# Kernel tuning notes

Measured on AMD Instinct MI355X. Metric: run time of the kernel, lower is better.

## Reference

```python
import jax, jax.numpy as jnp
import numpy as np

HIDDEN = 768
NUM_BLOCKS = 8
BLOCK = HIDDEN // NUM_BLOCKS
BASE_THR, K_DECAY, MIN_THR = 0.01, 20.0, 0.0005


def _threshold(height, width):
    # wavenumber-dependent soft-shrink threshold T(k), shape [H, W//2+1]
    fu = jnp.fft.fftfreq(height, d=1.0).astype(jnp.float32)[:, None]
    fv = jnp.fft.rfftfreq(width, d=1.0).astype(jnp.float32)[None, :]
    k = jnp.sqrt(fu ** 2 + fv ** 2) * max(height, width)
    thr = BASE_THR * jnp.exp(-0.5 * (k / K_DECAY) ** 2)
    return jnp.maximum(thr, MIN_THR)


def setup_inputs() -> dict:
    key = jax.random.key(0)
    kx, k1, k2, k3, k4 = jax.random.split(key, 5)
    scale = 0.02
    x = jax.random.normal(kx, (4, 128, 128, HIDDEN), dtype=jnp.float32)
    w1 = scale * jax.random.normal(k1, (2, NUM_BLOCKS, BLOCK, BLOCK), dtype=jnp.float32)
    b1 = scale * jax.random.normal(k2, (2, NUM_BLOCKS, BLOCK), dtype=jnp.float32)
    w2 = scale * jax.random.normal(k3, (2, NUM_BLOCKS, BLOCK, BLOCK), dtype=jnp.float32)
    b2 = scale * jax.random.normal(k4, (2, NUM_BLOCKS, BLOCK), dtype=jnp.float32)
    return {"x": x, "w1": w1, "b1": b1, "w2": w2, "b2": b2}


def reference(x, w1, b1, w2, b2):
    dtype = x.dtype
    bias = x
    xf = x.astype(jnp.float32)
    B, H, W, C = xf.shape
    Wc = W // 2 + 1
    # rfft2 over spatial dims, orthonormal
    Xc = jnp.fft.rfft2(xf, axes=(1, 2), norm='ortho')
    Xc = Xc.reshape(B, H, Wc, NUM_BLOCKS, BLOCK)
    xr, xi = jnp.real(Xc), jnp.imag(Xc)
    mm = lambda t, w: jnp.einsum('bhwni,nio->bhwno', t, w)
    # complex block-diagonal 2-layer MLP
    o1r = jax.nn.relu(mm(xr, w1[0]) - mm(xi, w1[1]) + b1[0])
    o1i = jax.nn.relu(mm(xi, w1[0]) + mm(xr, w1[1]) + b1[1])
    o2r = mm(o1r, w2[0]) - mm(o1i, w2[1]) + b2[0]
    o2i = mm(o1i, w2[0]) + mm(o1r, w2[1]) + b2[1]
    # soft-shrink on complex magnitude with wavenumber-dependent threshold
    mag = jnp.sqrt(o2r ** 2 + o2i ** 2 + 1e-8)
    thr = _threshold(H, W)[None, :, :, None, None]  # [1,H,Wc,1,1]
    sf = jax.nn.relu(mag - thr) / mag
    Yc = (o2r * sf) + 1j * (o2i * sf)
    Yc = Yc.reshape(B, H, Wc, C)
    y = jnp.fft.irfft2(Yc, s=(H, W), axes=(1, 2), norm='ortho')
    return y.astype(dtype) + bias
```

## Files before the change

### kernel.cpp

```cpp
#include <hip/hip_runtime.h>
#include <hip/hip_bf16.h>
#include <math.h>


#define HD   768
#define NBLK 8
#define HH   128
#define WW   128
#define WC   65
#define NPOS (HH * WC)

constexpr float SC    = 0.08838834764831845f;
constexpr float TWOPI = 6.28318530717958647692f;

constexpr int TM_OFF     = 0;
constexpr int TW_OFF     = 49152;
constexpr int TWI_OFF    = 69632;
constexpr int WF_OFF     = 90112;
constexpr int WF_END_U16 = 679936;
constexpr size_t A_UINTS = (size_t)4 * NPOS * HD;

typedef __attribute__((ext_vector_type(8))) short short8;
typedef __attribute__((ext_vector_type(4))) float f32x4;

#define MFMA __builtin_amdgcn_mfma_f32_16x16x32_bf16

static __device__ inline unsigned short f2bf(float f) {
  __hip_bfloat16 h = __float2bfloat16(f);
  return __builtin_bit_cast(unsigned short, h);
}
static __device__ inline unsigned int pack2(float re, float im) {
  return (unsigned int)f2bf(re) | ((unsigned int)f2bf(im) << 16);
}

__global__ __launch_bounds__(256) void k_prep(const float* __restrict__ w1,
                                              const float* __restrict__ b1,
                                              const float* __restrict__ w2,
                                              const float* __restrict__ b2,
                                              unsigned short* __restrict__ wf,
                                              float* __restrict__ bpk) {
  const int blk = blockIdx.x, t = threadIdx.x;
  if (blk < 16) {
    const int layer = blk >> 3, n = blk & 7;
    const float* w  = layer ? w2 : w1;
    const float* bs = layer ? b2 : b1;
    unsigned short* dst = wf + WF_OFF + (size_t)blk * (72 * 512);
    for (int e = t; e < 72 * 512; e += 256) {
      int f = e >> 9, idx = e & 511;
      int kk = f / 12, nt = f - kk * 12;
      int lane = idx >> 3, j = idx & 7;
      int k  = kk * 32 + (lane >> 4) * 8 + j;
      int cc = nt * 16 + (lane & 15);
      float v;
      if (k < 96) v = (cc < 96) ? w[(size_t)n * 9216 + k * 96 + cc]
                                : w[(size_t)(8 + n) * 9216 + k * 96 + (cc - 96)];
      else        v = (cc < 96) ? -w[(size_t)(8 + n) * 9216 + (k - 96) * 96 + cc]
                                :  w[(size_t)n * 9216 + (k - 96) * 96 + (cc - 96)];
      dst[e] = f2bf(v);
    }
    for (int c = t; c < 192; c += 256)
      bpk[blk * 192 + c] = (c < 96) ? bs[n * 96 + c] : bs[(8 + n) * 96 + (c - 96)];
  } else if (blk == 16) {
    for (int e = t; e < 96 * 512; e += 256) {
      int f = e >> 9, idx = e & 511;
      int part = f >> 5, rem = f & 31, kot = rem >> 2, kk = rem & 3;
      int lane = idx >> 3, j = idx & 7;
      int ko = kot * 16 + (lane & 15);
      int r  = kk * 32 + (lane >> 4) * 8 + j;
      float sn, cs; sincosf((TWOPI / 128.f) * (float)((ko * r) & 127), &sn, &cs);
      float v = (part == 0) ? cs : (part == 1) ? sn : -sn;
      wf[TM_OFF + (size_t)f * 512 + idx] = f2bf(v * SC);
    }
  } else if (blk == 17) {
    for (int e = t; e < 40 * 512; e += 256) {
      int f = e >> 9, idx = e & 511;
      int mt = f >> 2, kk = f & 3;
      int lane = idx >> 3, j = idx & 7;
      int row = mt * 16 + (lane & 15);
      int r   = kk * 32 + (lane >> 4) * 8 + j;
      int kor = (row < 80) ? row : row - 80;
      float sn, cs; sincosf((TWOPI / 128.f) * (float)((kor * r) & 127), &sn, &cs);
      wf[TW_OFF + (size_t)f * 512 + idx] = f2bf((row < 80 ? cs : -sn) * SC);
    }
  } else {
    for (int e = t; e < 40 * 512; e += 256) {
      int f = e >> 9, idx = e & 511;
      int mt = f / 5, kk = f - mt * 5;
      int lane = idx >> 3, j = idx & 7;
      int wr = mt * 16 + (lane & 15);
      int k  = kk * 32 + (lane >> 4) * 8 + j;
      float v = 0.f;
      if (k < 80) {
        int kb = k;
        if (kb <= 64) {
          float sn, cs; sincosf((TWOPI / 128.f) * (float)((wr * kb) & 127), &sn, &cs);
          v = SC * ((kb == 0 || kb == 64) ? 1.f : 2.f) * cs;
        }
      } else {
        int kb = k - 80;
        if (kb >= 1 && kb <= 63) {
          float sn, cs; sincosf((TWOPI / 128.f) * (float)((wr * kb) & 127), &sn, &cs);
          v = -2.f * SC * sn;
        }
      }
      wf[TWI_OFF + (size_t)f * 512 + idx] = f2bf(v);
    }
  }
}

__global__ __launch_bounds__(256) void k_fft_w(const float* __restrict__ x,
                                               unsigned int* __restrict__ A,
                                               const unsigned short* __restrict__ wf) {
  __shared__ unsigned short Xt[64 * 136];
  const int h = blockIdx.x, c0 = blockIdx.y * 64, b = blockIdx.z, t = threadIdx.x;
  const int wv = t >> 6, lane = t & 63, l15 = lane & 15, lg = lane >> 4;
  const float* xp = x + ((size_t)(b * HH + h)) * WW * HD + c0;
  for (int idx = t; idx < 128 * 64; idx += 256) {
    int r = idx >> 6, ch = idx & 63;
    Xt[ch * 136 + r] = f2bf(xp[(size_t)r * HD + ch]);
  }
  __syncthreads();
  const unsigned short* tw = wf + TW_OFF;
  f32x4 acc[10];
#pragma unroll
  for (int m = 0; m < 10; ++m) acc[m] = { 0.f, 0.f, 0.f, 0.f };
#pragma unroll
  for (int kk = 0; kk < 4; ++kk) {
    short8 bq = *(const short8*)&Xt[(wv * 16 + l15) * 136 + kk * 32 + lg * 8];
#pragma unroll
    for (int m = 0; m < 10; ++m) {
      short8 a = *(const short8*)&tw[(size_t)(m * 4 + kk) * 512 + lane * 8];
      acc[m] = MFMA(a, bq, acc[m], 0, 0, 0);
    }
  }
  unsigned int* Ao = A + ((size_t)b * NPOS + h * WC) * HD + c0 + wv * 16 + l15;
#pragma unroll
  for (int q = 0; q < 5; ++q)
#pragma unroll
    for (int r = 0; r < 4; ++r) {
      int ko = q * 16 + lg * 4 + r;
      if (ko <= 64) Ao[(size_t)ko * HD] = pack2(acc[q][r], acc[5 + q][r]);
    }
}

__global__ __launch_bounds__(256) void k_ifft_w(const unsigned int* __restrict__ A,
                                                const float* __restrict__ x,
                                                float* __restrict__ out,
                                                const unsigned short* __restrict__ wf) {
  __shared__ unsigned short Zt[64 * 168];
  const int h = blockIdx.x, c0 = blockIdx.y * 64, b = blockIdx.z, t = threadIdx.x;
  const int wv = t >> 6, lane = t & 63, l15 = lane & 15, lg = lane >> 4;
  const unsigned int* Ai = A + ((size_t)b * NPOS + h * WC) * HD + c0;
  for (int idx = t; idx < 65 * 64; idx += 256) {
    int kb = idx >> 6, ch = idx & 63;
    unsigned int u = Ai[(size_t)kb * HD + ch];
    Zt[ch * 168 + kb]      = (unsigned short)(u & 0xffffu);
    Zt[ch * 168 + 80 + kb] = (unsigned short)(u >> 16);
  }
  for (int idx = t; idx < 64 * 32; idx += 256) {
    int ch = idx >> 5, q = idx & 31;
    if (q < 30) {
      int kb = 65 + (q % 15), half = q / 15;
      Zt[ch * 168 + half * 80 + kb] = 0;
    }
  }
  __syncthreads();
  const unsigned short* twi = wf + TWI_OFF;
  f32x4 acc[8];
#pragma unroll
  for (int m = 0; m < 8; ++m) acc[m] = { 0.f, 0.f, 0.f, 0.f };
#pragma unroll
  for (int kk = 0; kk < 5; ++kk) {
    short8 bq = *(const short8*)&Zt[(wv * 16 + l15) * 168 + kk * 32 + lg * 8];
#pragma unroll
    for (int m = 0; m < 8; ++m) {
      short8 a = *(const short8*)&twi[(size_t)(m * 5 + kk) * 512 + lane * 8];
      acc[m] = MFMA(a, bq, acc[m], 0, 0, 0);
    }
  }
#pragma unroll
  for (int m = 0; m < 8; ++m)
#pragma unroll
    for (int r = 0; r < 4; ++r) {
      int wr = m * 16 + lg * 4 + r;
      size_t go = (((size_t)(b * HH + h)) * WW + wr) * HD + c0 + wv * 16 + l15;
      out[go] = acc[m][r] + x[go];
    }
}

template <int FWD>
static __device__ inline void dft_gemm16(const unsigned short* Rb, const unsigned short* Ib,
                                         const unsigned short* tm, int rt, int cb, int lane,
                                         f32x4* aR, f32x4* aI) {
  const int l15 = lane & 15, lg = lane >> 4;
#pragma unroll
  for (int kkr = 0; kkr < 4; ++kkr) {
    const int r0 = kkr * 32 + lg * 8;
    short8 Ac = *(const short8*)&tm[(size_t)(0 * 32 + rt * 4 + kkr) * 512 + lane * 8];
    short8 As = *(const short8*)&tm[(size_t)(1 * 32 + rt * 4 + kkr) * 512 + lane * 8];
    short8 An = *(const short8*)&tm[(size_t)(2 * 32 + rt * 4 + kkr) * 512 + lane * 8];
#pragma unroll
    for (int c = 0; c < 3; ++c) {
      short8 zr = *(const short8*)&Rb[((cb + c) * 16 + l15) * 136 + r0];
      short8 zi = *(const short8*)&Ib[((cb + c) * 16 + l15) * 136 + r0];
      aR[c] = MFMA(Ac, zr, aR[c], 0, 0, 0);
      if constexpr (FWD) {
        aR[c] = MFMA(As, zi, aR[c], 0, 0, 0);
        aI[c] = MFMA(Ac, zi, aI[c], 0, 0, 0);
        aI[c] = MFMA(An, zr, aI[c], 0, 0, 0);
      } else {
        aR[c] = MFMA(An, zi, aR[c], 0, 0, 0);
        aI[c] = MFMA(Ac, zi, aI[c], 0, 0, 0);
        aI[c] = MFMA(As, zr, aI[c], 0, 0, 0);
      }
    }
  }
}

__global__ __launch_bounds__(1024) void k_mid(unsigned int* __restrict__ A,
                                              const unsigned short* __restrict__ wf,
                                              const float* __restrict__ bpk) {
  __shared__ unsigned short Rb[13312], Ib[13312];
  __shared__ unsigned short WfL[36 * 512];
  const int kv = blockIdx.x, n = blockIdx.y, b = blockIdx.z, t = threadIdx.x;
  const int w = t >> 6, lane = t & 63, l15 = lane & 15, lg = lane >> 4;
  const int rt = w >> 1, cb = (w & 1) * 3;
  unsigned int* Abase = A + ((size_t)b * NPOS + kv) * HD + n * 96;
  const unsigned short* tm = wf + TM_OFF;

  for (int idx = t; idx < 128 * 96; idx += 1024) {
    int r = idx / 96, ch = idx - r * 96;
    unsigned int u = Abase[(size_t)r * (WC * HD) + ch];
    Rb[ch * 136 + r] = (unsigned short)(u & 0xffffu);
    Ib[ch * 136 + r] = (unsigned short)(u >> 16);
  }
  {
    const int4* s1 = (const int4*)(wf + WF_OFF + (size_t)n * (72 * 512));
    for (int idx = t; idx < 2304; idx += 1024) ((int4*)WfL)[idx] = s1[idx];
  }
  __syncthreads();

  f32x4 aR[3], aI[3];
#pragma unroll
  for (int c = 0; c < 3; ++c) { aR[c] = {0.f,0.f,0.f,0.f}; aI[c] = {0.f,0.f,0.f,0.f}; }
  dft_gemm16<1>(Rb, Ib, tm, rt, cb, lane, aR, aI);
  __syncthreads();
#pragma unroll
  for (int c = 0; c < 3; ++c)
#pragma unroll
    for (int r = 0; r < 4; ++r) {
      int row = rt * 16 + lg * 4 + r, ch = (cb + c) * 16 + l15;
      Rb[row * 104 + ch] = f2bf(aR[c][r]);
      Ib[row * 104 + ch] = f2bf(aI[c][r]);
    }
  __syncthreads();

  const int row_a = (rt * 16 + l15) * 104;
  f32x4 acc[6];
#pragma unroll
  for (int i = 0; i < 3; ++i) {
    float bv = bpk[n * 192 + (cb + i) * 16 + l15];
    acc[i] = { bv, bv, bv, bv };
    bv = bpk[n * 192 + (cb + i + 6) * 16 + l15];
    acc[3 + i] = { bv, bv, bv, bv };
  }
#pragma unroll
  for (int kk = 0; kk < 6; ++kk) {
    short8 a = (kk < 3) ? *(const short8*)&Rb[row_a + kk * 32 + lg * 8]
                        : *(const short8*)&Ib[row_a + (kk - 3) * 32 + lg * 8];
#pragma unroll
    for (int i = 0; i < 6; ++i) {
      int nt = cb + (i < 3 ? i : i + 3);
      short8 bfr;
      if (kk < 3) bfr = *(const short8*)&WfL[(kk * 12 + nt) * 512 + lane * 8];
      else {
        int nt2 = (nt < 6) ? nt + 6 : nt - 6;
        int4 nb = *(const int4*)&WfL[((kk - 3) * 12 + nt2) * 512 + lane * 8];
        if (nt < 6) { nb.x ^= 0x80008000; nb.y ^= 0x80008000; nb.z ^= 0x80008000; nb.w ^= 0x80008000; }
        bfr = __builtin_bit_cast(short8, nb);
      }
      acc[i] = MFMA(a, bfr, acc[i], 0, 0, 0);
    }
  }
  __syncthreads();
#pragma unroll
  for (int i = 0; i < 3; ++i)
#pragma unroll
    for (int r = 0; r < 4; ++r) {
      int row = rt * 16 + lg * 4 + r, ch = (cb + i) * 16 + l15;
      Rb[row * 104 + ch] = f2bf(fmaxf(acc[i][r], 0.f));
      Ib[row * 104 + ch] = f2bf(fmaxf(acc[3 + i][r], 0.f));
    }
  {
    const int4* s2 = (const int4*)(wf + WF_OFF + (size_t)(8 + n) * (72 * 512));
    for (int idx = t; idx < 2304; idx += 1024) ((int4*)WfL)[idx] = s2[idx];
  }
  __syncthreads();

#pragma unroll
  for (int i = 0; i < 3; ++i) {
    float bv = bpk[(8 + n) * 192 + (cb + i) * 16 + l15];
    acc[i] = { bv, bv, bv, bv };
    bv = bpk[(8 + n) * 192 + (cb + i + 6) * 16 + l15];
    acc[3 + i] = { bv, bv, bv, bv };
  }
#pragma unroll
  for (int kk = 0; kk < 6; ++kk) {
    short8 a = (kk < 3) ? *(const short8*)&Rb[row_a + kk * 32 + lg * 8]
                        : *(const short8*)&Ib[row_a + (kk - 3) * 32 + lg * 8];
#pragma unroll
    for (int i = 0; i < 6; ++i) {
      int nt = cb + (i < 3 ? i : i + 3);
      short8 bfr;
      if (kk < 3) bfr = *(const short8*)&WfL[(kk * 12 + nt) * 512 + lane * 8];
      else {
        int nt2 = (nt < 6) ? nt + 6 : nt - 6;
        int4 nb = *(const int4*)&WfL[((kk - 3) * 12 + nt2) * 512 + lane * 8];
        if (nt < 6) { nb.x ^= 0x80008000; nb.y ^= 0x80008000; nb.z ^= 0x80008000; nb.w ^= 0x80008000; }
        bfr = __builtin_bit_cast(short8, nb);
      }
      acc[i] = MFMA(a, bfr, acc[i], 0, 0, 0);
    }
  }
  __syncthreads();

#pragma unroll
  for (int r = 0; r < 4; ++r) {
    int ko = rt * 16 + lg * 4 + r;
    float kus = (ko >= 64) ? (float)(ko - 128) : (float)ko;
    float k2v = kus * kus + (float)(kv * kv);
    float thr = fmaxf(0.01f * expf(-0.00125f * k2v), 0.0005f);
#pragma unroll
    for (int i = 0; i < 3; ++i) {
      float mr = acc[i][r], mi = acc[3 + i][r];
      float mag = sqrtf(mr * mr + mi * mi + 1e-8f);
      float sf = fmaxf(mag - thr, 0.f) / mag;
      int ch = (cb + i) * 16 + l15;
      Rb[ch * 136 + ko] = f2bf(mr * sf);
      Ib[ch * 136 + ko] = f2bf(mi * sf);
    }
  }
  __syncthreads();

#pragma unroll
  for (int c = 0; c < 3; ++c) { aR[c] = {0.f,0.f,0.f,0.f}; aI[c] = {0.f,0.f,0.f,0.f}; }
  dft_gemm16<0>(Rb, Ib, tm, rt, cb, lane, aR, aI);
#pragma unroll
  for (int c = 0; c < 3; ++c)
#pragma unroll
    for (int r = 0; r < 4; ++r) {
      int rr = rt * 16 + lg * 4 + r, ch = (cb + c) * 16 + l15;
      Abase[(size_t)rr * (WC * HD) + ch] = pack2(aR[c][r], aI[c][r]);
    }
}

extern "C" void kernel_launch(void* const* d_in, const int* in_sizes, int n_in,
                              void* d_out, int out_size, void* d_ws, size_t ws_size,
                              hipStream_t stream) {
  const float* x  = (const float*)d_in[0];
  const float* w1 = (const float*)d_in[1];
  const float* b1 = (const float*)d_in[2];
  const float* w2 = (const float*)d_in[3];
  const float* b2 = (const float*)d_in[4];
  float* out = (float*)d_out;
  unsigned int* A = (unsigned int*)d_ws;

  unsigned short* wf = (unsigned short*)(A + A_UINTS);
  float* bpk = (float*)(wf + WF_END_U16);

  k_prep<<<19, 256, 0, stream>>>(w1, b1, w2, b2, wf, bpk);
  k_fft_w<<<dim3(HH, HD / 64, 4), 256, 0, stream>>>(x, A, wf);
  k_mid<<<dim3(WC, NBLK, 4), 1024, 0, stream>>>(A, wf, bpk);
  k_ifft_w<<<dim3(HH, HD / 64, 4), 256, 0, stream>>>(A, x, out, wf);
}
```

Baseline: 462.3 us.

## Fold residual add into spectrum and double-buffer MLP weight tiles in k_mid

The residual x is no longer read in fp32 at the inverse FFT. Instead k_mid writes its filtered spectrum to a separate buffer, and k_ifft_w adds it to the stored forward spectrum of x before the inverse transform. This uses linearity of the orthonormal rfft/irfft pair and saves a full-size fp32 read of x, at the cost of one extra bf16-complex read and reconstructing x from a bf16 spectrum, which can lose accuracy. k_mid also streams its MLP weights through two 12-tile LDS buffers overlapped with compute, instead of loading all 36 tiles up front. It packs pairs of rows into 32-bit LDS stores and adds a launch-bounds occupancy hint.

```diff
diff --git a/kernel.cpp b/kernel.cpp
--- a/kernel.cpp
+++ b/kernel.cpp
@@ -31,6 +31,12 @@
 }
 static __device__ inline unsigned int pack2(float re, float im) {
   return (unsigned int)f2bf(re) | ((unsigned int)f2bf(im) << 16);
+}
+static __device__ inline float lo2f(unsigned int u) {
+  return __builtin_bit_cast(float, u << 16);
+}
+static __device__ inline float hi2f(unsigned int u) {
+  return __builtin_bit_cast(float, u & 0xffff0000u);
 }
 
 __global__ __launch_bounds__(256) void k_prep(const float* __restrict__ w1,
@@ -144,18 +150,21 @@
 }
 
 __global__ __launch_bounds__(256) void k_ifft_w(const unsigned int* __restrict__ A,
-                                                const float* __restrict__ x,
+                                                const unsigned int* __restrict__ Bp,
                                                 float* __restrict__ out,
                                                 const unsigned short* __restrict__ wf) {
   __shared__ unsigned short Zt[64 * 168];
   const int h = blockIdx.x, c0 = blockIdx.y * 64, b = blockIdx.z, t = threadIdx.x;
   const int wv = t >> 6, lane = t & 63, l15 = lane & 15, lg = lane >> 4;
-  const unsigned int* Ai = A + ((size_t)b * NPOS + h * WC) * HD + c0;
+  const size_t base = ((size_t)b * NPOS + h * WC) * HD + c0;
   for (int idx = t; idx < 65 * 64; idx += 256) {
     int kb = idx >> 6, ch = idx & 63;
-    unsigned int u = Ai[(size_t)kb * HD + ch];
-    Zt[ch * 168 + kb]      = (unsigned short)(u & 0xffffu);
-    Zt[ch * 168 + 80 + kb] = (unsigned short)(u >> 16);
+    unsigned int uA = A[base + (size_t)kb * HD + ch];
+    unsigned int uB = Bp[base + (size_t)kb * HD + ch];
+    float re = lo2f(uA) + lo2f(uB);
+    float im = hi2f(uA) + hi2f(uB);
+    Zt[ch * 168 + kb]      = f2bf(re);
+    Zt[ch * 168 + 80 + kb] = (kb == 0 || kb == 64) ? (unsigned short)0 : f2bf(im);
   }
   for (int idx = t; idx < 64 * 32; idx += 256) {
     int ch = idx >> 5, q = idx & 31;
@@ -184,7 +193,7 @@
     for (int r = 0; r < 4; ++r) {
       int wr = m * 16 + lg * 4 + r;
       size_t go = (((size_t)(b * HH + h)) * WW + wr) * HD + c0 + wv * 16 + l15;
-      out[go] = acc[m][r] + x[go];
+      out[go] = acc[m][r];
     }
 }
 
@@ -217,26 +226,31 @@
   }
 }
 
-__global__ __launch_bounds__(1024) void k_mid(unsigned int* __restrict__ A,
-                                              const unsigned short* __restrict__ wf,
-                                              const float* __restrict__ bpk) {
+__global__ __launch_bounds__(1024, 8) void k_mid(const unsigned int* __restrict__ A,
+                                                 unsigned int* __restrict__ Bp,
+                                                 const unsigned short* __restrict__ wf,
+                                                 const float* __restrict__ bpk) {
   __shared__ unsigned short Rb[13312], Ib[13312];
-  __shared__ unsigned short WfL[36 * 512];
+  __shared__ unsigned short WfX[2][12 * 512];
   const int kv = blockIdx.x, n = blockIdx.y, b = blockIdx.z, t = threadIdx.x;
   const int w = t >> 6, lane = t & 63, l15 = lane & 15, lg = lane >> 4;
   const int rt = w >> 1, cb = (w & 1) * 3;
-  unsigned int* Abase = A + ((size_t)b * NPOS + kv) * HD + n * 96;
+  const size_t pbase = ((size_t)b * NPOS + kv) * HD + n * 96;
   const unsigned short* tm = wf + TM_OFF;
-
-  for (int idx = t; idx < 128 * 96; idx += 1024) {
-    int r = idx / 96, ch = idx - r * 96;
-    unsigned int u = Abase[(size_t)r * (WC * HD) + ch];
-    Rb[ch * 136 + r] = (unsigned short)(u & 0xffffu);
-    Ib[ch * 136 + r] = (unsigned short)(u >> 16);
-  }
+  const unsigned short* wf1 = wf + WF_OFF + (size_t)n * (72 * 512);
+  const unsigned short* wf2 = wf + WF_OFF + (size_t)(8 + n) * (72 * 512);
+
   {
-    const int4* s1 = (const int4*)(wf + WF_OFF + (size_t)n * (72 * 512));
-    for (int idx = t; idx < 2304; idx += 1024) ((int4*)WfL)[idx] = s1[idx];
+    unsigned int* Rb32 = (unsigned int*)Rb;
+    unsigned int* Ib32 = (unsigned int*)Ib;
+    for (int idx = t; idx < 64 * 96; idx += 1024) {
+      int r2 = idx / 96, ch = idx - r2 * 96;
+      unsigned int u0 = A[pbase + (size_t)(2 * r2) * (WC * HD) + ch];
+      unsigned int u1 = A[pbase + (size_t)(2 * r2 + 1) * (WC * HD) + ch];
+      Rb32[ch * 68 + r2] = (u0 & 0xffffu) | (u1 << 16);
+      Ib32[ch * 68 + r2] = (u0 >> 16) | (u1 & 0xffff0000u);
+    }
+    if (t < 768) ((int4*)WfX[0])[t] = ((const int4*)(wf1 + 0 * 12 * 512))[t];
   }
   __syncthreads();
 
@@ -244,7 +258,9 @@
 #pragma unroll
   for (int c = 0; c < 3; ++c) { aR[c] = {0.f,0.f,0.f,0.f}; aI[c] = {0.f,0.f,0.f,0.f}; }
   dft_gemm16<1>(Rb, Ib, tm, rt, cb, lane, aR, aI);
-  __syncthreads();
+  if (t < 768) ((int4*)WfX[1])[t] = ((const int4*)(wf1 + 1 * 12 * 512))[t];
+  __syncthreads();
+
 #pragma unroll
   for (int c = 0; c < 3; ++c)
 #pragma unroll
@@ -264,25 +280,33 @@
     bv = bpk[n * 192 + (cb + i + 6) * 16 + l15];
     acc[3 + i] = { bv, bv, bv, bv };
   }
-#pragma unroll
-  for (int kk = 0; kk < 6; ++kk) {
-    short8 a = (kk < 3) ? *(const short8*)&Rb[row_a + kk * 32 + lg * 8]
-                        : *(const short8*)&Ib[row_a + (kk - 3) * 32 + lg * 8];
-#pragma unroll
-    for (int i = 0; i < 6; ++i) {
-      int nt = cb + (i < 3 ? i : i + 3);
-      short8 bfr;
-      if (kk < 3) bfr = *(const short8*)&WfL[(kk * 12 + nt) * 512 + lane * 8];
-      else {
-        int nt2 = (nt < 6) ? nt + 6 : nt - 6;
-        int4 nb = *(const int4*)&WfL[((kk - 3) * 12 + nt2) * 512 + lane * 8];
-        if (nt < 6) { nb.x ^= 0x80008000; nb.y ^= 0x80008000; nb.z ^= 0x80008000; nb.w ^= 0x80008000; }
-        bfr = __builtin_bit_cast(short8, nb);
-      }
-      acc[i] = MFMA(a, bfr, acc[i], 0, 0, 0);
-    }
-  }
-  __syncthreads();
+
+#define MLP_PAIR(k0, BUF)                                                        \
+  {                                                                              \
+    short8 aRf = *(const short8*)&Rb[row_a + (k0) * 32 + lg * 8];                \
+    short8 aIf = *(const short8*)&Ib[row_a + (k0) * 32 + lg * 8];                \
+    _Pragma("unroll")                                                            \
+    for (int i = 0; i < 6; ++i) {                                                \
+      int nt = cb + (i < 3 ? i : i + 3);                                         \
+      short8 b0 = *(const short8*)&(BUF)[nt * 512 + lane * 8];                   \
+      acc[i] = MFMA(aRf, b0, acc[i], 0, 0, 0);                                   \
+      int nt2 = (nt < 6) ? nt + 6 : nt - 6;                                      \
+      int4 nb = *(const int4*)&(BUF)[nt2 * 512 + lane * 8];                      \
+      if (nt < 6) { nb.x ^= 0x80008000; nb.y ^= 0x80008000;                      \
+                    nb.z ^= 0x80008000; nb.w ^= 0x80008000; }                    \
+      acc[i] = MFMA(aIf, __builtin_bit_cast(short8, nb), acc[i], 0, 0, 0);       \
+    }                                                                            \
+  }
+
+  MLP_PAIR(0, WfX[0]);
+  __syncthreads();
+  MLP_PAIR(1, WfX[1]);
+  if (t < 768) ((int4*)WfX[0])[t] = ((const int4*)(wf1 + 2 * 12 * 512))[t];
+  __syncthreads();
+  MLP_PAIR(2, WfX[0]);
+  if (t < 768) ((int4*)WfX[1])[t] = ((const int4*)(wf2 + 0 * 12 * 512))[t];
+  __syncthreads();
+
 #pragma unroll
   for (int i = 0; i < 3; ++i)
 #pragma unroll
@@ -291,10 +315,7 @@
       Rb[row * 104 + ch] = f2bf(fmaxf(acc[i][r], 0.f));
       Ib[row * 104 + ch] = f2bf(fmaxf(acc[3 + i][r], 0.f));
     }
-  {
-    const int4* s2 = (const int4*)(wf + WF_OFF + (size_t)(8 + n) * (72 * 512));
-    for (int idx = t; idx < 2304; idx += 1024) ((int4*)WfL)[idx] = s2[idx];
-  }
+  if (t < 768) ((int4*)WfX[0])[t] = ((const int4*)(wf2 + 1 * 12 * 512))[t];
   __syncthreads();
 
 #pragma unroll
@@ -304,24 +325,12 @@
     bv = bpk[(8 + n) * 192 + (cb + i + 6) * 16 + l15];
     acc[3 + i] = { bv, bv, bv, bv };
   }
-#pragma unroll
-  for (int kk = 0; kk < 6; ++kk) {
-    short8 a = (kk < 3) ? *(const short8*)&Rb[row_a + kk * 32 + lg * 8]
-                        : *(const short8*)&Ib[row_a + (kk - 3) * 32 + lg * 8];
-#pragma unroll
-    for (int i = 0; i < 6; ++i) {
-      int nt = cb + (i < 3 ? i : i + 3);
-      short8 bfr;
-      if (kk < 3) bfr = *(const short8*)&WfL[(kk * 12 + nt) * 512 + lane * 8];
-      else {
-        int nt2 = (nt < 6) ? nt + 6 : nt - 6;
-        int4 nb = *(const int4*)&WfL[((kk - 3) * 12 + nt2) * 512 + lane * 8];
-        if (nt < 6) { nb.x ^= 0x80008000; nb.y ^= 0x80008000; nb.z ^= 0x80008000; nb.w ^= 0x80008000; }
-        bfr = __builtin_bit_cast(short8, nb);
-      }
-      acc[i] = MFMA(a, bfr, acc[i], 0, 0, 0);
-    }
-  }
+  MLP_PAIR(0, WfX[1]);
+  __syncthreads();
+  MLP_PAIR(1, WfX[0]);
+  if (t < 768) ((int4*)WfX[1])[t] = ((const int4*)(wf2 + 2 * 12 * 512))[t];
+  __syncthreads();
+  MLP_PAIR(2, WfX[1]);
   __syncthreads();
 
 #pragma unroll
@@ -350,8 +359,9 @@
 #pragma unroll
     for (int r = 0; r < 4; ++r) {
       int rr = rt * 16 + lg * 4 + r, ch = (cb + c) * 16 + l15;
-      Abase[(size_t)rr * (WC * HD) + ch] = pack2(aR[c][r], aI[c][r]);
-    }
+      Bp[pbase + (size_t)rr * (WC * HD) + ch] = pack2(aR[c][r], aI[c][r]);
+    }
+#undef MLP_PAIR
 }
 
 extern "C" void kernel_launch(void* const* d_in, const int* in_sizes, int n_in,
@@ -363,13 +373,14 @@
   const float* w2 = (const float*)d_in[3];
   const float* b2 = (const float*)d_in[4];
   float* out = (float*)d_out;
-  unsigned int* A = (unsigned int*)d_ws;
-
-  unsigned short* wf = (unsigned short*)(A + A_UINTS);
+  unsigned int* A  = (unsigned int*)d_ws;
+  unsigned int* Bp = A + A_UINTS;
+
+  unsigned short* wf = (unsigned short*)(Bp + A_UINTS);
   float* bpk = (float*)(wf + WF_END_U16);
 
   k_prep<<<19, 256, 0, stream>>>(w1, b1, w2, b2, wf, bpk);
   k_fft_w<<<dim3(HH, HD / 64, 4), 256, 0, stream>>>(x, A, wf);
-  k_mid<<<dim3(WC, NBLK, 4), 1024, 0, stream>>>(A, wf, bpk);
-  k_ifft_w<<<dim3(HH, HD / 64, 4), 256, 0, stream>>>(A, x, out, wf);
-}
+  k_mid<<<dim3(WC, NBLK, 4), 1024, 0, stream>>>(A, Bp, wf, bpk);
+  k_ifft_w<<<dim3(HH, HD / 64, 4), 256, 0, stream>>>(A, Bp, out, wf);
+}
```

Result: no change. 468.9 us (+1.4%).
